# Optimization experiments

Measured on AMD Instinct MI355X. Metric: run time of the kernel, lower is better.

Reference implementation:

```python
import jax, jax.numpy as jnp
import numpy as np

TEMP = 1.0


def _layernorm(x):
    # mean/std over last dim; torch.std is unbiased (ddof=1); no eps in original
    x = x - jnp.mean(x, axis=-1, keepdims=True)
    return x / jnp.std(x, axis=-1, keepdims=True, ddof=1)


def setup_inputs() -> dict:
    key = jax.random.key(0)
    ks = jax.random.split(key, 5)
    B, S, d_in, d = 8, 2048, 768, 1024
    return {
        "seq": jax.random.normal(ks[0], (B, S, d_in), dtype=jnp.float32),
        "embedding": jax.random.normal(ks[1], (d_in, d), dtype=jnp.float32),
        "W1": jax.random.normal(ks[2], (d, d), dtype=jnp.float32),
        "W2": jax.random.normal(ks[3], (d, d), dtype=jnp.float32),
        "readout": jax.random.normal(ks[4], (d,), dtype=jnp.float32),
    }


def reference(seq, embedding, W1, W2, readout):
    d_in = seq.shape[-1]
    d = embedding.shape[-1]
    x = jnp.matmul(seq, embedding) / jnp.sqrt(jnp.float32(d_in))  # [B,S,d]
    # depth == 1: single block
    gram = jnp.einsum("bsd,btd->bst", x, x) / x.shape[-1]  # [B,S,S]
    weights = jax.nn.softmax(gram / TEMP, axis=-1)
    post_attn = _layernorm(x + jnp.matmul(weights, x))  # [B,S,d]
    h = jnp.matmul(post_attn, W1) / jnp.sqrt(jnp.float32(d))
    h = jnp.matmul(jax.nn.relu(h), W2) / jnp.sqrt(jnp.float32(d))
    x = _layernorm(h + post_attn)
    pooled = jnp.mean(x, axis=1)  # [B,d]
    out = jnp.matmul(pooled, readout) / jnp.sqrt(jnp.float32(d))  # [B]
    return out
```

## Files before the change

### kernel.cpp

```cpp
#include <hip/hip_runtime.h>
#include <hip/hip_bf16.h>

typedef __bf16 bf16x8 __attribute__((ext_vector_type(8)));
typedef float f32x4 __attribute__((ext_vector_type(4)));

__device__ __forceinline__ unsigned short f2bf(float f) {
  union { float f; unsigned u; } x; x.f = f;
  unsigned r = x.u + 0x7fffu + ((x.u >> 16) & 1u);
  return (unsigned short)(r >> 16);
}
__device__ __forceinline__ float bf2f(unsigned short u) {
  union { unsigned u; float f; } x; x.u = (unsigned)u << 16;
  return x.f;
}
__device__ __forceinline__ unsigned short f2h(float f) {
  union { _Float16 h; unsigned short u; } x; x.h = (_Float16)f;
  return x.u;
}
__device__ __forceinline__ float h2f(unsigned short u) {
  union { _Float16 h; unsigned short u; } x; x.u = u;
  return (float)x.h;
}

__device__ __forceinline__ void async_ld16(const void* g, void* l) {
  __builtin_amdgcn_global_load_lds(
      (__attribute__((address_space(1))) void*)const_cast<void*>(g),
      (__attribute__((address_space(3))) void*)l, 16, 0, 0);
}


#define EPI_F32    0
#define EPI_BF     1
#define EPI_RELUBF 2
#define EPI_F16    3

__global__ __launch_bounds__(512, 2) void gemm_bt(
    const unsigned short* __restrict__ A,
    const unsigned short* __restrict__ Bt,
    int M, int N, int K, int nbatch,
    long sA, long sB, long sC,
    float scale, int mode, void* __restrict__ outp)
{
  __shared__ unsigned short lds[65536];
  const int t = threadIdx.x;
  const int w = t >> 6, l = t & 63;
  const int lr = l & 15, lg = l >> 4;
  const int wr = w >> 2, wc = w & 3;
  const int ntn = N >> 8;
  const int tiles = (M >> 8) * ntn;
  const int chunk = (tiles * nbatch) >> 3;
  const int bid = blockIdx.x;
  const int wg = (bid & 7) * chunk + (bid >> 3);
  const int batch = wg / tiles;
  const int rem = wg - batch * tiles;
  const int row0 = (rem / ntn) << 8;
  const int col0 = (rem % ntn) << 8;

  const unsigned short* Ab  = A  + (long)batch * sA;
  const unsigned short* Btb = Bt + (long)batch * sB;

  const int rsub = t >> 3;
  const int cg8  = ((t & 7) ^ (rsub & 7)) << 3;
  const long arow = (long)(row0 + rsub) * K;
  const long brow = (long)(col0 + rsub) * K;
  const long rstep = (long)K << 6;

  const int NT = K >> 6;

#define STAGE(buf, kk0)                                                     \
  {                                                                         \
    const unsigned short* sa = Ab + arow + (kk0) + cg8;                     \
    const unsigned short* sb = Btb + brow + (kk0) + cg8;                    \
    unsigned short* da = (buf) + t * 8;                                     \
    unsigned short* db = (buf) + 16384 + t * 8;                             \
    async_ld16(sa,             da);                                         \
    async_ld16(sa + rstep,     da + 4096);                                  \
    async_ld16(sa + 2 * rstep, da + 8192);                                  \
    async_ld16(sa + 3 * rstep, da + 12288);                                 \
    async_ld16(sb,             db);                                         \
    async_ld16(sb + rstep,     db + 4096);                                  \
    async_ld16(sb + 2 * rstep, db + 8192);                                  \
    async_ld16(sb + 3 * rstep, db + 12288);                                 \
  }

  f32x4 acc[8][4];
#pragma unroll
  for (int m = 0; m < 8; ++m)
#pragma unroll
    for (int n = 0; n < 4; ++n) acc[m][n] = (f32x4){0.f, 0.f, 0.f, 0.f};

  STAGE(lds, 0);
  __builtin_amdgcn_sched_barrier(0);

  for (int tt = 0; tt < NT; ++tt) {
    unsigned short* ldsA = lds + (tt & 1) * 32768;
    unsigned short* ldsB = ldsA + 16384;
    unsigned short* ldsN = lds + ((tt + 1) & 1) * 32768;

    __builtin_amdgcn_s_barrier();
    __builtin_amdgcn_sched_barrier(0);
    if (tt + 1 < NT) {
      STAGE(ldsN, (tt + 1) << 6);
      __builtin_amdgcn_sched_barrier(0);
      asm volatile("s_waitcnt vmcnt(8)" ::: "memory");
    } else {
      asm volatile("s_waitcnt vmcnt(0)" ::: "memory");
    }
    __builtin_amdgcn_sched_barrier(0);
    __builtin_amdgcn_s_barrier();
    __builtin_amdgcn_sched_barrier(0);

#pragma unroll
    for (int kk = 0; kk < 2; ++kk) {
      bf16x8 af[8], bfr[4];
#pragma unroll
      for (int mf = 0; mf < 8; ++mf) {
        int Ra = wr * 128 + mf * 16 + lr;
        af[mf] = *(const bf16x8*)&ldsA[Ra * 64 + ((kk * 32 + lg * 8) ^ ((Ra & 7) << 3))];
      }
#pragma unroll
      for (int nf = 0; nf < 4; ++nf) {
        int Rb = wc * 64 + nf * 16 + lr;
        bfr[nf] = *(const bf16x8*)&ldsB[Rb * 64 + ((kk * 32 + lg * 8) ^ ((Rb & 7) << 3))];
      }
      __builtin_amdgcn_s_setprio(1);
#pragma unroll
      for (int mf = 0; mf < 8; ++mf)
#pragma unroll
        for (int nf = 0; nf < 4; ++nf)
          acc[mf][nf] = __builtin_amdgcn_mfma_f32_16x16x32_bf16(af[mf], bfr[nf], acc[mf][nf], 0, 0, 0);
      __builtin_amdgcn_s_setprio(0);
    }
    __builtin_amdgcn_sched_barrier(0);
  }

  float* outF = (float*)outp;
  unsigned short* outH = (unsigned short*)outp;
  const size_t cb = (size_t)batch * (size_t)sC;
#pragma unroll
  for (int mf = 0; mf < 8; ++mf) {
    int rbase = row0 + wr * 128 + mf * 16 + lg * 4;
#pragma unroll
    for (int nf = 0; nf < 4; ++nf) {
      int c = col0 + wc * 64 + nf * 16 + lr;
      f32x4 v = acc[mf][nf];
#pragma unroll
      for (int q = 0; q < 4; ++q) {
        size_t idx = cb + (size_t)(rbase + q) * N + c;
        float val = v[q] * scale;
        if (mode == EPI_F32)         outF[idx] = val;
        else if (mode == EPI_BF)     outH[idx] = f2bf(val);
        else if (mode == EPI_RELUBF) outH[idx] = f2bf(fmaxf(val, 0.f));
        else                         outH[idx] = f2h(val);
      }
    }
  }
#undef STAGE
}


__device__ __forceinline__ float wave_sum(float v) {
#pragma unroll
  for (int o = 32; o; o >>= 1) v += __shfl_xor(v, o, 64);
  return v;
}
__device__ __forceinline__ float wave_max(float v) {
#pragma unroll
  for (int o = 32; o; o >>= 1) v = fmaxf(v, __shfl_xor(v, o, 64));
  return v;
}

__global__ __launch_bounds__(256) void cast_bf16(const float* __restrict__ in,
                                                 unsigned short* __restrict__ out, long n) {
  long i = ((long)blockIdx.x * 256 + threadIdx.x) * 4;
  if (i >= n) return;
  float4 v = *(const float4*)&in[i];
  ushort4 o;
  o.x = f2bf(v.x); o.y = f2bf(v.y); o.z = f2bf(v.z); o.w = f2bf(v.w);
  *(ushort4*)&out[i] = o;
}

__global__ __launch_bounds__(256) void transpose_cast(const float* __restrict__ in,
                                                      unsigned short* __restrict__ out,
                                                      int R, int C) {
  __shared__ float tile[32][33];
  int c0 = blockIdx.x * 32, r0 = blockIdx.y * 32;
  int tx = threadIdx.x, ty = threadIdx.y;
  for (int i = ty; i < 32; i += 8) tile[i][tx] = in[(size_t)(r0 + i) * C + c0 + tx];
  __syncthreads();
  for (int i = ty; i < 32; i += 8) out[(size_t)(c0 + i) * R + r0 + tx] = f2bf(tile[tx][i]);
}

__global__ __launch_bounds__(256) void transpose_b16(const unsigned short* __restrict__ in,
                                                     unsigned short* __restrict__ out,
                                                     int R, int C) {
  __shared__ unsigned short tile[32][33];
  int c0 = blockIdx.x * 32, r0 = blockIdx.y * 32;
  size_t zb = (size_t)blockIdx.z * R * C;
  int tx = threadIdx.x, ty = threadIdx.y;
  for (int i = ty; i < 32; i += 8) tile[i][tx] = in[zb + (size_t)(r0 + i) * C + c0 + tx];
  __syncthreads();
  for (int i = ty; i < 32; i += 8) out[zb + (size_t)(c0 + i) * R + r0 + tx] = tile[tx][i];
}

__global__ __launch_bounds__(256) void softmax_rows(const unsigned short* __restrict__ g,
                                                    unsigned short* __restrict__ wout) {
  __shared__ float red[4];
  int row = blockIdx.x, t = threadIdx.x;
  const unsigned short* gr = g + ((size_t)row << 11) + t * 8;
  ushort4 ua = *(const ushort4*)gr;
  ushort4 ub = *(const ushort4*)(gr + 4);
  float a0 = h2f(ua.x), a1 = h2f(ua.y), a2 = h2f(ua.z), a3 = h2f(ua.w);
  float b0 = h2f(ub.x), b1 = h2f(ub.y), b2 = h2f(ub.z), b3 = h2f(ub.w);
  float mx = fmaxf(fmaxf(fmaxf(a0, a1), fmaxf(a2, a3)),
                   fmaxf(fmaxf(b0, b1), fmaxf(b2, b3)));
  mx = wave_max(mx);
  if ((t & 63) == 0) red[t >> 6] = mx;
  __syncthreads();
  mx = fmaxf(fmaxf(red[0], red[1]), fmaxf(red[2], red[3]));
  float e0 = __expf(a0 - mx), e1 = __expf(a1 - mx), e2 = __expf(a2 - mx), e3 = __expf(a3 - mx);
  float e4 = __expf(b0 - mx), e5 = __expf(b1 - mx), e6 = __expf(b2 - mx), e7 = __expf(b3 - mx);
  float s = ((e0 + e1) + (e2 + e3)) + ((e4 + e5) + (e6 + e7));
  s = wave_sum(s);
  __syncthreads();
  if ((t & 63) == 0) red[t >> 6] = s;
  __syncthreads();
  s = (red[0] + red[1]) + (red[2] + red[3]);
  float inv = 1.0f / s;
  ushort4 o0, o1;
  o0.x = f2bf(e0 * inv); o0.y = f2bf(e1 * inv); o0.z = f2bf(e2 * inv); o0.w = f2bf(e3 * inv);
  o1.x = f2bf(e4 * inv); o1.y = f2bf(e5 * inv); o1.z = f2bf(e6 * inv); o1.w = f2bf(e7 * inv);
  size_t base = ((size_t)row << 11) + t * 8;
  *(ushort4*)&wout[base] = o0;
  *(ushort4*)&wout[base + 4] = o1;
}

__global__ __launch_bounds__(256) void ln_residual_bf(const unsigned short* __restrict__ xb,
                                                      const float* __restrict__ attn,
                                                      unsigned short* __restrict__ outB) {
  __shared__ float red[4];
  int row = blockIdx.x, t = threadIdx.x;
  size_t base = ((size_t)row << 10) + t * 4;
  ushort4 ua = *(const ushort4*)&xb[base];
  float4 vb = *(const float4*)&attn[base];
  float4 v = {bf2f(ua.x) + vb.x, bf2f(ua.y) + vb.y, bf2f(ua.z) + vb.z, bf2f(ua.w) + vb.w};
  float s = (v.x + v.y) + (v.z + v.w);
  float ss = (v.x * v.x + v.y * v.y) + (v.z * v.z + v.w * v.w);
  s = wave_sum(s);
  if ((t & 63) == 0) red[t >> 6] = s;
  __syncthreads();
  s = (red[0] + red[1]) + (red[2] + red[3]);
  ss = wave_sum(ss);
  __syncthreads();
  if ((t & 63) == 0) red[t >> 6] = ss;
  __syncthreads();
  ss = (red[0] + red[1]) + (red[2] + red[3]);
  float mean = s * (1.0f / 1024.0f);
  float var = (ss - s * mean) * (1.0f / 1023.0f);
  float rstd = rsqrtf(var);
  ushort4 ob;
  ob.x = f2bf((v.x - mean) * rstd); ob.y = f2bf((v.y - mean) * rstd);
  ob.z = f2bf((v.z - mean) * rstd); ob.w = f2bf((v.w - mean) * rstd);
  *(ushort4*)&outB[base] = ob;
}

__global__ __launch_bounds__(256) void ln_residual_dot(const unsigned short* __restrict__ h2,
                                                       const unsigned short* __restrict__ post,
                                                       const float* __restrict__ readout,
                                                       float* __restrict__ rowdot) {
  __shared__ float red[4];
  int row = blockIdx.x, t = threadIdx.x;
  size_t base = ((size_t)row << 10) + t * 4;
  ushort4 ua = *(const ushort4*)&h2[base];
  ushort4 ub = *(const ushort4*)&post[base];
  float4 v = {bf2f(ua.x) + bf2f(ub.x), bf2f(ua.y) + bf2f(ub.y),
              bf2f(ua.z) + bf2f(ub.z), bf2f(ua.w) + bf2f(ub.w)};
  float s = (v.x + v.y) + (v.z + v.w);
  float ss = (v.x * v.x + v.y * v.y) + (v.z * v.z + v.w * v.w);
  s = wave_sum(s);
  if ((t & 63) == 0) red[t >> 6] = s;
  __syncthreads();
  s = (red[0] + red[1]) + (red[2] + red[3]);
  ss = wave_sum(ss);
  __syncthreads();
  if ((t & 63) == 0) red[t >> 6] = ss;
  __syncthreads();
  ss = (red[0] + red[1]) + (red[2] + red[3]);
  float mean = s * (1.0f / 1024.0f);
  float var = (ss - s * mean) * (1.0f / 1023.0f);
  float rstd = rsqrtf(var);
  float4 r = *(const float4*)&readout[t * 4];
  float dot = (v.x - mean) * rstd * r.x + (v.y - mean) * rstd * r.y +
              (v.z - mean) * rstd * r.z + (v.w - mean) * rstd * r.w;
  dot = wave_sum(dot);
  __syncthreads();
  if ((t & 63) == 0) red[t >> 6] = dot;
  __syncthreads();
  if (t == 0) rowdot[row] = (red[0] + red[1]) + (red[2] + red[3]);
}

__global__ __launch_bounds__(256) void reduce_out(const float* __restrict__ rowdot,
                                                  float* __restrict__ out) {
  __shared__ float red[4];
  int b = blockIdx.x, t = threadIdx.x;
  float s = 0.f;
  for (int i = t; i < 2048; i += 256) s += rowdot[(size_t)b * 2048 + i];
  s = wave_sum(s);
  if ((t & 63) == 0) red[t >> 6] = s;
  __syncthreads();
  if (t == 0) out[b] = ((red[0] + red[1]) + (red[2] + red[3])) * (1.0f / 65536.0f);
}

extern "C" void kernel_launch(void* const* d_in, const int* in_sizes, int n_in,
                              void* d_out, int out_size, void* d_ws, size_t ws_size,
                              hipStream_t stream) {
  const float* seq     = (const float*)d_in[0];
  const float* emb     = (const float*)d_in[1];
  const float* W1      = (const float*)d_in[2];
  const float* W2      = (const float*)d_in[3];
  const float* readout = (const float*)d_in[4];
  float* out = (float*)d_out;

  char* ws = (char*)d_ws;
  const size_t MB = 1024u * 1024u;
  unsigned short* x_b    = (unsigned short*)(ws + 0);
  unsigned short* h2b    = (unsigned short*)(ws + 0);
  unsigned short* xT     = (unsigned short*)(ws + 32 * MB);
  unsigned short* hrelu  = (unsigned short*)(ws + 32 * MB);
  unsigned short* gram   = (unsigned short*)(ws + 64 * MB);
  float*          attn   = (float*)(ws + 64 * MB);
  unsigned short* wts    = (unsigned short*)(ws + 128 * MB);
  unsigned short* post_b = (unsigned short*)(ws + 128 * MB);
  unsigned short* seq_b  = (unsigned short*)(ws + 192 * MB);
  unsigned short* embT   = (unsigned short*)(ws + 216 * MB);
  unsigned short* W1T    = (unsigned short*)(ws + 218 * MB);
  unsigned short* W2T    = (unsigned short*)(ws + 220 * MB);
  float*          rowdot = (float*)(ws + 222 * MB);

  cast_bf16<<<12288, 256, 0, stream>>>(seq, seq_b, 12582912L);
  transpose_cast<<<dim3(32, 24), dim3(32, 8), 0, stream>>>(emb, embT, 768, 1024);
  transpose_cast<<<dim3(32, 32), dim3(32, 8), 0, stream>>>(W1, W1T, 1024, 1024);
  transpose_cast<<<dim3(32, 32), dim3(32, 8), 0, stream>>>(W2, W2T, 1024, 1024);

  gemm_bt<<<256, 512, 0, stream>>>(seq_b, embT, 16384, 1024, 768, 1, 0, 0, 0,
                                   0.03608439182435161f, EPI_BF, x_b);

  transpose_b16<<<dim3(32, 64, 8), dim3(32, 8), 0, stream>>>(x_b, xT, 2048, 1024);

  gemm_bt<<<512, 512, 0, stream>>>(x_b, x_b, 2048, 2048, 1024, 8,
                                   2048L * 1024, 2048L * 1024, 2048L * 2048,
                                   1.0f / 1024.0f, EPI_F16, gram);

  softmax_rows<<<16384, 256, 0, stream>>>(gram, wts);

  gemm_bt<<<256, 512, 0, stream>>>(wts, xT, 2048, 1024, 2048, 8,
                                   2048L * 2048, 1024L * 2048, 2048L * 1024,
                                   1.0f, EPI_F32, attn);

  ln_residual_bf<<<16384, 256, 0, stream>>>(x_b, attn, post_b);

  gemm_bt<<<256, 512, 0, stream>>>(post_b, W1T, 16384, 1024, 1024, 1, 0, 0, 0,
                                   0.03125f, EPI_RELUBF, hrelu);
  gemm_bt<<<256, 512, 0, stream>>>(hrelu, W2T, 16384, 1024, 1024, 1, 0, 0, 0,
                                   0.03125f, EPI_BF, h2b);

  ln_residual_dot<<<16384, 256, 0, stream>>>(h2b, post_b, readout, rowdot);
  reduce_out<<<8, 256, 0, stream>>>(rowdot, out);
}
```

Measured before the change: 393.9 us.

## Split GEMM k-tile into half-stages and interleave async loads with MFMA

Restructures the bf16 GEMM main loop so each 64-wide k-tile is staged as two 32-wide halves with a new LDS layout and XOR swizzle. Global-to-LDS async loads for the next tile are issued between fragment reads and MFMA groups, with finer-grained waitcnt/barriers per half. The aim is to hide load latency behind compute and cut register pressure from af fragments, at the cost of more barriers per tile and a new, riskier swizzle layout.

```diff
diff --git a/kernel.cpp b/kernel.cpp
--- a/kernel.cpp
+++ b/kernel.cpp
@@ -59,29 +59,19 @@
   const unsigned short* Ab  = A  + (long)batch * sA;
   const unsigned short* Btb = Bt + (long)batch * sB;
 
-  const int rsub = t >> 3;
-  const int cg8  = ((t & 7) ^ (rsub & 7)) << 3;
-  const long arow = (long)(row0 + rsub) * K;
-  const long brow = (long)(col0 + rsub) * K;
-  const long rstep = (long)K << 6;
+  const int ks = ((lg ^ ((lr >> 1) & 3)) << 3);
+
+  const int srow = w * 16 + (l >> 2);
+  const int kgo  = (((l & 3) ^ ((l >> 3) & 3)) << 3);
+  const long aoff0 = (long)(row0 + srow) * K + kgo;
+  const long boff0 = (long)(col0 + srow) * K + kgo;
+  const long off128 = (long)K << 7;
 
   const int NT = K >> 6;
 
-#define STAGE(buf, kk0)                                                     \
-  {                                                                         \
-    const unsigned short* sa = Ab + arow + (kk0) + cg8;                     \
-    const unsigned short* sb = Btb + brow + (kk0) + cg8;                    \
-    unsigned short* da = (buf) + t * 8;                                     \
-    unsigned short* db = (buf) + 16384 + t * 8;                             \
-    async_ld16(sa,             da);                                         \
-    async_ld16(sa + rstep,     da + 4096);                                  \
-    async_ld16(sa + 2 * rstep, da + 8192);                                  \
-    async_ld16(sa + 3 * rstep, da + 12288);                                 \
-    async_ld16(sb,             db);                                         \
-    async_ld16(sb + rstep,     db + 4096);                                  \
-    async_ld16(sb + 2 * rstep, db + 8192);                                  \
-    async_ld16(sb + 3 * rstep, db + 12288);                                 \
-  }
+#define STAGEP(partE, base, kcol)                                      \
+  { async_ld16((base) + (kcol),          &lds[(partE) + t * 8]);       \
+    async_ld16((base) + off128 + (kcol), &lds[(partE) + 4096 + t * 8]); }
 
   f32x4 acc[8][4];
 #pragma unroll
@@ -89,49 +79,69 @@
 #pragma unroll
     for (int n = 0; n < 4; ++n) acc[m][n] = (f32x4){0.f, 0.f, 0.f, 0.f};
 
-  STAGE(lds, 0);
+  STAGEP(0,     Btb + boff0, 0);
+  STAGEP(8192,  Ab + aoff0,  0);
+  STAGEP(16384, Btb + boff0, 32);
+  STAGEP(24576, Ab + aoff0,  32);
   __builtin_amdgcn_sched_barrier(0);
 
   for (int tt = 0; tt < NT; ++tt) {
-    unsigned short* ldsA = lds + (tt & 1) * 32768;
-    unsigned short* ldsB = ldsA + 16384;
-    unsigned short* ldsN = lds + ((tt + 1) & 1) * 32768;
-
-    __builtin_amdgcn_s_barrier();
-    __builtin_amdgcn_sched_barrier(0);
-    if (tt + 1 < NT) {
-      STAGE(ldsN, (tt + 1) << 6);
+    const int bufe  = (tt & 1) << 15;
+    const int nbufe = ((tt + 1) & 1) << 15;
+    const bool st = (tt + 1) < NT;
+    const int kn = (tt + 1) << 6;
+
+#pragma unroll
+    for (int kh = 0; kh < 2; ++kh) {
+      if (kh == 0 || st) { asm volatile("s_waitcnt vmcnt(4)" ::: "memory"); }
+      else               { asm volatile("s_waitcnt vmcnt(0)" ::: "memory"); }
       __builtin_amdgcn_sched_barrier(0);
-      asm volatile("s_waitcnt vmcnt(8)" ::: "memory");
-    } else {
-      asm volatile("s_waitcnt vmcnt(0)" ::: "memory");
+      __builtin_amdgcn_s_barrier();
+      __builtin_amdgcn_sched_barrier(0);
+
+      const int pB = bufe + kh * 16384;
+      const int pA = pB + 8192;
+
+      bf16x8 bfr[4];
+#pragma unroll
+      for (int nf = 0; nf < 4; ++nf) {
+        int rb = wc * 64 + nf * 16 + lr;
+        bfr[nf] = *(const bf16x8*)&lds[pB + rb * 32 + ks];
+      }
+      {
+        bf16x8 af[4];
+#pragma unroll
+        for (int i = 0; i < 4; ++i) {
+          int ra = wr * 128 + i * 16 + lr;
+          af[i] = *(const bf16x8*)&lds[pA + ra * 32 + ks];
+        }
+        if (st) STAGEP(nbufe + kh * 16384, Btb + boff0, kn + kh * 32);
+        __builtin_amdgcn_s_setprio(1);
+#pragma unroll
+        for (int i = 0; i < 4; ++i)
+#pragma unroll
+          for (int nf = 0; nf < 4; ++nf)
+            acc[i][nf] = __builtin_amdgcn_mfma_f32_16x16x32_bf16(af[i], bfr[nf], acc[i][nf], 0, 0, 0);
+        __builtin_amdgcn_s_setprio(0);
+      }
+      {
+        bf16x8 af[4];
+#pragma unroll
+        for (int i = 0; i < 4; ++i) {
+          int ra = wr * 128 + 64 + i * 16 + lr;
+          af[i] = *(const bf16x8*)&lds[pA + ra * 32 + ks];
+        }
+        if (st) STAGEP(nbufe + kh * 16384 + 8192, Ab + aoff0, kn + kh * 32);
+        __builtin_amdgcn_s_setprio(1);
+#pragma unroll
+        for (int i = 0; i < 4; ++i)
+#pragma unroll
+          for (int nf = 0; nf < 4; ++nf)
+            acc[4 + i][nf] = __builtin_amdgcn_mfma_f32_16x16x32_bf16(af[i], bfr[nf], acc[4 + i][nf], 0, 0, 0);
+        __builtin_amdgcn_s_setprio(0);
+      }
+      __builtin_amdgcn_sched_barrier(0);
     }
-    __builtin_amdgcn_sched_barrier(0);
-    __builtin_amdgcn_s_barrier();
-    __builtin_amdgcn_sched_barrier(0);
-
-#pragma unroll
-    for (int kk = 0; kk < 2; ++kk) {
-      bf16x8 af[8], bfr[4];
-#pragma unroll
-      for (int mf = 0; mf < 8; ++mf) {
-        int Ra = wr * 128 + mf * 16 + lr;
-        af[mf] = *(const bf16x8*)&ldsA[Ra * 64 + ((kk * 32 + lg * 8) ^ ((Ra & 7) << 3))];
-      }
-#pragma unroll
-      for (int nf = 0; nf < 4; ++nf) {
-        int Rb = wc * 64 + nf * 16 + lr;
-        bfr[nf] = *(const bf16x8*)&ldsB[Rb * 64 + ((kk * 32 + lg * 8) ^ ((Rb & 7) << 3))];
-      }
-      __builtin_amdgcn_s_setprio(1);
-#pragma unroll
-      for (int mf = 0; mf < 8; ++mf)
-#pragma unroll
-        for (int nf = 0; nf < 4; ++nf)
-          acc[mf][nf] = __builtin_amdgcn_mfma_f32_16x16x32_bf16(af[mf], bfr[nf], acc[mf][nf], 0, 0, 0);
-      __builtin_amdgcn_s_setprio(0);
-    }
-    __builtin_amdgcn_sched_barrier(0);
   }
 
   float* outF = (float*)outp;
@@ -155,7 +165,7 @@
       }
     }
   }
-#undef STAGE
+#undef STAGEP
 }
 
 
```

After: 385.2 us. 1.02x faster.
